# Optimization experiments

Measured on AMD Instinct MI355X. Metric: run time of the kernel, lower is better.

The kernel has to match this reference:

```python
import jax, jax.numpy as jnp
import numpy as np

ALPHA = 0.5
BETA = 0.25
D_AGG = 0.5          # delta_aggregation
D_DIS = 3.0          # delta_discrimination
OHEM_RATIO = 3.0
MAX_INST = 8         # max instance label (labels in 1..MAX_INST, 0 = background)
SMOOTH = 1e-3


def _aggr_discr(text, kernel, embed):
    # text, kernel: [HW] int32 instance labels; embed: [4, HW] float
    inst = jnp.arange(1, MAX_INST + 1)                              # [I]
    kmask = (kernel[None, :] == inst[:, None]).astype(embed.dtype)  # [I, HW]
    tmask = (text[None, :] == inst[:, None]).astype(embed.dtype)   # [I, HW]
    kcnt = kmask.sum(1)                                             # [I]
    tcnt = tmask.sum(1)
    valid = ((kcnt > 0) & (tcnt > 0)).astype(embed.dtype)           # [I]
    # per-instance kernel-mean embedding (segment mean)
    avgs = (kmask @ embed.T) / jnp.maximum(kcnt, 1.0)[:, None]      # [I, 4]
    # aggregation: per-pixel distance to the mean of its text instance
    avgs_full = jnp.concatenate([jnp.zeros((1, 4), embed.dtype), avgs], 0)  # row 0 = bg
    pix_avg = avgs_full[text]                                       # [HW, 4]
    sq = jnp.sum((embed.T - pix_avg) ** 2, axis=1)
    dist = jnp.sqrt(sq + 1e-12) - D_AGG
    lg = jnp.log1p(jnp.maximum(dist, 0.0) ** 2)                     # [HW]
    aggr_i = (tmask @ lg) / jnp.maximum(tcnt, 1.0)                  # [I]
    n = valid.sum()
    loss_aggr = jnp.where(n > 0, (aggr_i * valid).sum() / jnp.maximum(n, 1.0), 0.0)
    # discrimination: pairwise hinge between valid kernel means
    pairv = jnp.triu(valid[:, None] * valid[None, :], k=1)          # [I, I]
    sq_ij = jnp.sum((avgs[:, None, :] - avgs[None, :, :]) ** 2, axis=-1)
    d_ij = jnp.sqrt(jnp.where(pairv > 0, sq_ij, 1.0))               # safe sqrt
    L = jnp.log1p(jnp.maximum(D_DIS - d_ij, 0.0) ** 2)
    denom = n * (n - 1)
    loss_discr = jnp.where(n > 1, (L * pairv).sum() / jnp.maximum(denom, 1.0), 0.0)
    return loss_aggr, loss_discr


def _ohem(score, gt_text, gt_mask):
    # score, gt_text, gt_mask: [HW] float
    pos = gt_text > 0.5
    maskpos = gt_mask > 0.5
    pos_num = (pos & maskpos).sum()
    neg = ~pos
    neg_num = jnp.minimum((pos_num * OHEM_RATIO).astype(jnp.int32), neg.sum())
    neg_sc = jnp.where(neg, score, -jnp.inf)
    srt = -jnp.sort(-neg_sc)                                        # descending
    thr = srt[jnp.clip(neg_num - 1, 0, score.shape[0] - 1)]
    samp = ((score >= thr) | pos) & maskpos
    fallback = (pos_num == 0) | (neg_num == 0)
    return jnp.where(fallback, maskpos, samp).astype(score.dtype)


def _dice(pred_logits, target, mask):
    # all [N, HW]
    p = jax.nn.sigmoid(pred_logits) * mask
    t = (target > 0.5).astype(p.dtype) * mask
    a = jnp.sum(p * t, 1) + SMOOTH
    b = jnp.sum(p * p, 1) + SMOOTH
    c = jnp.sum(t * t, 1) + SMOOTH
    return 1.0 - 2.0 * a / (b + c)


def reference(preds, gt_texts, gt_kernels, gt_mask):
    N, C, H, W = preds.shape
    HW = H * W
    pred_text = preds[:, 0].reshape(N, HW)
    pred_kernel = preds[:, 1].reshape(N, HW)
    embed = preds[:, 2:].reshape(N, 4, HW)
    t = gt_texts.reshape(N, HW)
    k = gt_kernels.reshape(N, HW)
    m = gt_mask.reshape(N, HW).astype(preds.dtype)
    tf = t.astype(preds.dtype)
    kf = k.astype(preds.dtype)
    loss_aggr, loss_discr = jax.vmap(_aggr_discr)(t, k, embed)
    samp = jax.vmap(_ohem)(jax.lax.stop_gradient(pred_text), tf, m)
    loss_text = _dice(pred_text, tf, samp)
    samp_k = (tf > 0.5).astype(preds.dtype) * m
    loss_kernel = _dice(pred_kernel, kf, samp_k)
    # reduction='mean' then coefs [1, alpha, beta, beta]
    return jnp.stack([
        loss_text.mean(),
        ALPHA * loss_kernel.mean(),
        BETA * loss_aggr.mean(),
        BETA * loss_discr.mean(),
    ])


def setup_inputs() -> dict:
    key = jax.random.key(0)
    k1, k2, k3, k4 = jax.random.split(key, 4)
    N, H, W = 16, 512, 512
    preds = jax.random.normal(k1, (N, 6, H, W), dtype=jnp.float32)
    gt_texts = jax.random.randint(k2, (N, H, W), 0, 9, dtype=jnp.int32)
    gt_kernels = jax.random.randint(k3, (N, H, W), 0, 9, dtype=jnp.int32)
    gt_mask = jax.random.randint(k4, (N, H, W), 0, 2, dtype=jnp.int32)
    return {"preds": preds, "gt_texts": gt_texts, "gt_kernels": gt_kernels, "gt_mask": gt_mask}
```

## Files before the change

### kernel.cpp

```cpp
#include <hip/hip_runtime.h>
#include <math.h>

#define HW (512 * 512)
#define NB 16
#define NTHR 256
#define GXS 64
#define CH 4
#define NSEG 256
#define SEGSZ 1024
#define REP 16

#define OFF_ACC    0
#define ACC_STRIDE (NB * 52)
#define OFF_PACC   (OFF_ACC + REP * ACC_STRIDE)
#define PACC_STRIDE (NB * 4)
#define OFF_HISTFB (OFF_PACC + REP * PACC_STRIDE)
#define OFF_NEGMX  (OFF_HISTFB + 4 * 16 * 256)
#define ZERO_WORDS (OFF_NEGMX + NB * REP)
#define OFF_TBL    ZERO_WORDS
#define OFF_THR    (OFF_TBL + 16 * 45)
#define OFF_FB     (OFF_THR + 16)
#define OFF_NVAL   (OFF_FB + 16)
#define OFF_DISCR  (OFF_NVAL + 16)
#define OFF_PREFIX (OFF_DISCR + 16)
#define OFF_KKC    (OFF_PREFIX + 16)
#define OFF_NEGC   (OFF_KKC + 16)
#define OFF_CNTS   (OFF_NEGC + 16)
#define OFF_KEYS   (OFF_CNTS + NB * NSEG)
#define WS_FULL_BYTES ((size_t)(OFF_KEYS + NB * HW) * 4)


__device__ __forceinline__ unsigned fmap(float f) {
    unsigned u = __float_as_uint(f);
    return (u & 0x80000000u) ? ~u : (u | 0x80000000u);
}
__device__ __forceinline__ float funmap(unsigned u) {
    return (u & 0x80000000u) ? __uint_as_float(u & 0x7FFFFFFFu)
                             : __uint_as_float(~u);
}
__device__ __forceinline__ float wred(float x) {
#pragma unroll
    for (int o = 32; o; o >>= 1) x += __shfl_xor(x, o);
    return x;
}
__device__ __forceinline__ unsigned wredu(unsigned x) {
#pragma unroll
    for (int o = 32; o; o >>= 1) x += __shfl_xor(x, o);
    return x;
}
__device__ __forceinline__ unsigned wredumax(unsigned x) {
#pragma unroll
    for (int o = 32; o; o >>= 1) x = max(x, (unsigned)__shfl_xor((int)x, o));
    return x;
}

__global__ __launch_bounds__(NTHR, 2) void k_stats(const float* __restrict__ preds,
                        const int* __restrict__ text,
                        const int* __restrict__ kern,
                        const int* __restrict__ mask,
                        unsigned* __restrict__ wsu, int do_compact) {
    float* wsf = (float*)wsu;
    const int b = blockIdx.y;
    const int tid = threadIdx.x;
    const int lane = tid & 63;
    const unsigned long long lmask = (1ull << lane) - 1ull;
    __shared__ float sacc[52];
    if (tid < 52) sacc[tid] = 0.f;
    __syncthreads();

    const int* tb = text + b * HW;
    const int* kb = kern + b * HW;
    const int* mb = mask + b * HW;
    const float* p0 = preds + (size_t)(b * 6 + 0) * HW;
    const float* p1 = preds + (size_t)(b * 6 + 1) * HW;
    const float* e0 = preds + (size_t)(b * 6 + 2) * HW;
    const float* e1 = e0 + HW;
    const float* e2 = e0 + 2 * HW;
    const float* e3 = e0 + 3 * HW;

    const int seg = blockIdx.x * 4 + (tid >> 6);
    unsigned* keys = wsu + OFF_KEYS + (size_t)b * HW + (size_t)seg * SEGSZ;
    unsigned segoff = 0;
    unsigned mkAll = 0u;

    float ks[32];
#pragma unroll
    for (int i = 0; i < 32; i++) ks[i] = 0.f;
    float r_ak = 0.f, r_bk = 0.f, r_ck = 0.f;
    unsigned kcW[8] = {0, 0, 0, 0, 0, 0, 0, 0};
    unsigned tcW[8] = {0, 0, 0, 0, 0, 0, 0, 0};
    unsigned posW = 0;

#pragma unroll 1
    for (int c = 0; c < CH; c++) {
        const int base = blockIdx.x * (NTHR * 4 * CH) + c * (NTHR * 4) + tid * 4;
        const int4 t4 = *(const int4*)(tb + base);
        const int4 k4 = *(const int4*)(kb + base);
        const int4 m4 = *(const int4*)(mb + base);
        const float4 s4 = *(const float4*)(p0 + base);
        const float4 q4 = *(const float4*)(p1 + base);
        const float4 a4 = *(const float4*)(e0 + base);
        const float4 b4 = *(const float4*)(e1 + base);
        const float4 c4 = *(const float4*)(e2 + base);
        const float4 d4 = *(const float4*)(e3 + base);

#define PIX(T, K, M, Q, A, B, C, D) do {                                     \
        bool pos_ = (T) > 0, mp_ = (M) > 0;                                  \
        float sm_ = (pos_ && mp_) ? 1.f : 0.f;                               \
        float sg_ = 1.f / (1.f + expf(-(Q)));                                \
        float ik_ = ((K) > 0) ? 1.f : 0.f;                                   \
        r_ak += sm_ * sg_ * ik_;                                             \
        r_bk += sm_ * sg_ * sg_;                                             \
        r_ck += sm_ * ik_;                                                   \
        posW += (unsigned)__popcll(__ballot(pos_ && mp_));                   \
        _Pragma("unroll")                                                    \
        for (int i_ = 0; i_ < 8; i_++) {                                     \
            bool hit_ = ((K) == i_ + 1);                                     \
            kcW[i_] += (unsigned)__popcll(__ballot(hit_));                   \
            tcW[i_] += (unsigned)__popcll(__ballot((T) == i_ + 1));          \
            float h_ = hit_ ? 1.f : 0.f;                                     \
            ks[i_ * 4 + 0] += h_ * (A);                                      \
            ks[i_ * 4 + 1] += h_ * (B);                                      \
            ks[i_ * 4 + 2] += h_ * (C);                                      \
            ks[i_ * 4 + 3] += h_ * (D);                                      \
        }                                                                    \
    } while (0)

        PIX(t4.x, k4.x, m4.x, q4.x, a4.x, b4.x, c4.x, d4.x);
        PIX(t4.y, k4.y, m4.y, q4.y, a4.y, b4.y, c4.y, d4.y);
        PIX(t4.z, k4.z, m4.z, q4.z, a4.z, b4.z, c4.z, d4.z);
        PIX(t4.w, k4.w, m4.w, q4.w, a4.w, b4.w, c4.w, d4.w);
#undef PIX

        const unsigned long long m0 = __ballot(t4.x == 0);
        const unsigned long long m1 = __ballot(t4.y == 0);
        const unsigned long long m2 = __ballot(t4.z == 0);
        const unsigned long long m3 = __ballot(t4.w == 0);
        const unsigned c0 = (unsigned)__popcll(m0), c1 = (unsigned)__popcll(m1);
        const unsigned c2 = (unsigned)__popcll(m2), c3 = (unsigned)__popcll(m3);
        if (do_compact) {
            if (t4.x == 0) keys[segoff + (unsigned)__popcll(m0 & lmask)] = fmap(s4.x);
            if (t4.y == 0) keys[segoff + c0 + (unsigned)__popcll(m1 & lmask)] = fmap(s4.y);
            if (t4.z == 0) keys[segoff + c0 + c1 + (unsigned)__popcll(m2 & lmask)] = fmap(s4.z);
            if (t4.w == 0) keys[segoff + c0 + c1 + c2 + (unsigned)__popcll(m3 & lmask)] = fmap(s4.w);
        }
        segoff += c0 + c1 + c2 + c3;
        unsigned mk = 0u;
        if (t4.x == 0) mk = max(mk, ~fmap(s4.x));
        if (t4.y == 0) mk = max(mk, ~fmap(s4.y));
        if (t4.z == 0) mk = max(mk, ~fmap(s4.z));
        if (t4.w == 0) mk = max(mk, ~fmap(s4.w));
        mkAll = max(mkAll, mk);
    }

    if (lane == 0) wsu[OFF_CNTS + b * NSEG + seg] = segoff;
    mkAll = wredumax(mkAll);
    if (lane == 0 && mkAll)
        atomicMax(&wsu[OFF_NEGMX + b * REP + (blockIdx.x & (REP - 1))], mkAll);

#pragma unroll
    for (int i = 0; i < 32; i++) {
        float v = wred(ks[i]);
        if (lane == 0) atomicAdd(&sacc[16 + i], v);
    }
    {
        float v = wred(r_ak); if (lane == 0) atomicAdd(&sacc[49], v);
        v = wred(r_bk); if (lane == 0) atomicAdd(&sacc[50], v);
        v = wred(r_ck); if (lane == 0) atomicAdd(&sacc[51], v);
    }
    if (lane == 0) {
#pragma unroll
        for (int i = 0; i < 8; i++) {
            atomicAdd(&sacc[i], (float)kcW[i]);
            atomicAdd(&sacc[8 + i], (float)tcW[i]);
        }
        atomicAdd(&sacc[48], (float)posW);
    }
    __syncthreads();
    if (tid < 52) {
        const int rep = blockIdx.x & (REP - 1);
        atomicAdd(&wsf[OFF_ACC + rep * ACC_STRIDE + b * 52 + tid], sacc[tid]);
    }
}

__global__ void k_sel(unsigned* __restrict__ wsu, int do_select) {
    float* wsf = (float*)wsu;
    const int b = blockIdx.x;
    const int tid = threadIdx.x;
    const int lane = tid & 63;
    __shared__ float s_acc[52];
    __shared__ float s_avg[8][4];
    __shared__ int s_valid[8];
    __shared__ unsigned s_hist[256];
    __shared__ unsigned s_negtot;
    __shared__ unsigned s_kk, s_prefix;

    if (tid < 52) {
        float v = 0.f;
#pragma unroll
        for (int r = 0; r < REP; r++) v += wsf[OFF_ACC + r * ACC_STRIDE + b * 52 + tid];
        s_acc[tid] = v;
    }
    if (tid == 0) s_negtot = 0u;
    __syncthreads();

    const unsigned myc = wsu[OFF_CNTS + b * NSEG + tid];
    {
        unsigned cw = wredu(myc);
        if (lane == 0) atomicAdd(&s_negtot, cw);
    }
    if (tid < 8) {
        float kcf = s_acc[tid];
        float tcf = s_acc[8 + tid];
        int valid = (kcf > 0.f && tcf > 0.f) ? 1 : 0;
        float inv = 1.f / fmaxf(kcf, 1.f);
        float w = valid ? 1.f / fmaxf(tcf, 1.f) : 0.f;
#pragma unroll
        for (int c = 0; c < 4; c++) {
            float a = s_acc[16 + tid * 4 + c] * inv;
            s_avg[tid][c] = a;
            wsf[OFF_TBL + b * 45 + (tid + 1) * 5 + c] = a;
        }
        s_valid[tid] = valid;
        wsf[OFF_TBL + b * 45 + (tid + 1) * 5 + 4] = w;
    }
    if (tid >= 8 && tid < 13) wsf[OFF_TBL + b * 45 + (tid - 8)] = 0.f;
    __syncthreads();
    if (tid == 0) {
        int nval = 0;
        for (int i = 0; i < 8; i++) nval += s_valid[i];
        float L = 0.f;
        for (int i = 0; i < 8; i++)
            for (int j = i + 1; j < 8; j++)
                if (s_valid[i] && s_valid[j]) {
                    float sq = 0.f;
                    for (int c = 0; c < 4; c++) {
                        float d = s_avg[i][c] - s_avg[j][c];
                        sq += d * d;
                    }
                    float h = fmaxf(3.0f - sqrtf(sq), 0.f);
                    L += log1pf(h * h);
                }
        wsf[OFF_DISCR + b] = (nval > 1) ? L / fmaxf((float)(nval * (nval - 1)), 1.f) : 0.f;
        wsu[OFF_NVAL + b] = (unsigned)nval;
        unsigned pos = (unsigned)s_acc[48];
        unsigned neg = s_negtot;
        wsu[OFF_NEGC + b] = neg;
        unsigned nn = min(pos * 3u, neg);
        int fb = (pos == 0u || nn == 0u) ? 1 : 0;
        wsu[OFF_FB + b] = (unsigned)fb;
        wsu[OFF_KKC + b] = fb ? 0u : nn;
        wsu[OFF_PREFIX + b] = 0u;
        wsf[OFF_THR + b] = 0.f;
        unsigned kk = fb ? 0u : nn;
        if (!fb && nn == neg) {
            unsigned mx = 0u;
#pragma unroll
            for (int r = 0; r < REP; r++) mx = max(mx, wsu[OFF_NEGMX + b * REP + r]);
            wsf[OFF_THR + b] = funmap(~mx);
            kk = 0u;
        }
        s_kk = kk;
        s_prefix = 0u;
    }
    __syncthreads();
    if (!do_select) return;
    if (s_kk == 0u) return;
    const unsigned* keys = wsu + OFF_KEYS + (size_t)b * HW + (size_t)tid * SEGSZ;
    unsigned prefix = 0u;
    for (int pass = 0; pass < 4; pass++) {
        const int shift = 24 - 8 * pass;
        const unsigned fmask = (pass == 0) ? 0u : (0xFFFFFFFFu << (shift + 8));
        s_hist[tid] = 0u;
        __syncthreads();
        for (unsigned i = 0; i < myc; i++) {
            unsigned key = keys[i];
            if ((key & fmask) == prefix) atomicAdd(&s_hist[(key >> shift) & 255u], 1u);
        }
        __syncthreads();
        if (tid == 0) {
            unsigned k2 = s_kk;
            for (int bin = 255; bin >= 0; --bin) {
                unsigned c = s_hist[bin];
                if (k2 <= c) { s_prefix = prefix | (((unsigned)bin) << shift); s_kk = k2; break; }
                k2 -= c;
            }
        }
        __syncthreads();
        prefix = s_prefix;
    }
    if (tid == 0) wsf[OFF_THR + b] = funmap(prefix);
}

__global__ void k_hist(const float* __restrict__ preds, const int* __restrict__ text,
                       unsigned* __restrict__ wsu, int pass) {
    const int b = blockIdx.y;
    const int tid = threadIdx.x;
    __shared__ unsigned h[256];
    h[tid] = 0u;
    __syncthreads();
    const unsigned prefix = wsu[OFF_PREFIX + b];
    const int shift = 24 - 8 * pass;
    const unsigned fmask = (pass == 0) ? 0u : (0xFFFFFFFFu << (shift + 8));
    const int* tb = text + b * HW;
    const float* pt = preds + (size_t)(b * 6) * HW;
    for (int p = blockIdx.x * NTHR + tid; p < HW; p += gridDim.x * NTHR) {
        if (tb[p] == 0) {
            unsigned key = fmap(pt[p]);
            if ((key & fmask) == prefix) atomicAdd(&h[(key >> shift) & 255u], 1u);
        }
    }
    __syncthreads();
    if (h[tid]) atomicAdd(&wsu[OFF_HISTFB + pass * 4096 + b * 256 + tid], h[tid]);
}
__global__ void k_select(unsigned* __restrict__ wsu, int pass) {
    int b = threadIdx.x;
    if (b >= NB) return;
    float* wsf = (float*)wsu;
    unsigned k = wsu[OFF_KKC + b];
    unsigned prefix = wsu[OFF_PREFIX + b];
    const int shift = 24 - 8 * pass;
    const unsigned* h = &wsu[OFF_HISTFB + pass * 4096 + b * 256];
    if (k > 0) {
        for (int bin = 255; bin >= 0; --bin) {
            unsigned c = h[bin];
            if (k <= c) { prefix |= ((unsigned)bin) << shift; break; }
            k -= c;
        }
        wsu[OFF_KKC + b] = k;
        wsu[OFF_PREFIX + b] = prefix;
    }
    if (pass == 3) wsf[OFF_THR + b] = funmap(prefix);
}

__global__ __launch_bounds__(NTHR, 2) void k_pix(const float* __restrict__ preds,
                      const int* __restrict__ text,
                      const int* __restrict__ mask,
                      unsigned* __restrict__ wsu) {
    float* wsf = (float*)wsu;
    const int b = blockIdx.y;
    const int tid = threadIdx.x;
    const int lane = tid & 63;
    __shared__ float stbl[45];
    __shared__ float sred[4];
    __shared__ float sthr;
    __shared__ unsigned sfb;
    if (tid < 45) stbl[tid] = wsf[OFF_TBL + b * 45 + tid];
    if (tid < 4) sred[tid] = 0.f;
    if (tid == 0) { sthr = wsf[OFF_THR + b]; sfb = wsu[OFF_FB + b]; }
    __syncthreads();
    const float thr = sthr;
    const bool fb = sfb != 0u;
    float r_at = 0.f, r_bt = 0.f, r_ct = 0.f, r_ag = 0.f;
    const int* tb = text + b * HW;
    const int* mb = mask + b * HW;
    const float* p0 = preds + (size_t)(b * 6) * HW;
    const float* e0 = preds + (size_t)(b * 6 + 2) * HW;
    const float* e1 = e0 + HW;
    const float* e2 = e0 + 2 * HW;
    const float* e3 = e0 + 3 * HW;

#pragma unroll 1
    for (int c = 0; c < CH; c++) {
        const int base = blockIdx.x * (NTHR * 4 * CH) + c * (NTHR * 4) + tid * 4;
        const int4 t4 = *(const int4*)(tb + base);
        const int4 m4 = *(const int4*)(mb + base);
        const float4 s4 = *(const float4*)(p0 + base);
        const float4 a4 = *(const float4*)(e0 + base);
        const float4 b4 = *(const float4*)(e1 + base);
        const float4 c4 = *(const float4*)(e2 + base);
        const float4 d4 = *(const float4*)(e3 + base);

#define PPIX(T, M, S, A, B, C, D) do {                                       \
        bool pos_ = (T) > 0;                                                 \
        bool samp_ = fb ? ((M) > 0) : ((((S) >= thr) || pos_) && ((M) > 0)); \
        float sg_ = 1.f / (1.f + expf(-(S)));                                \
        float smf_ = samp_ ? 1.f : 0.f;                                      \
        float it_ = pos_ ? 1.f : 0.f;                                        \
        r_at += smf_ * sg_ * it_;                                            \
        r_bt += smf_ * sg_ * sg_;                                            \
        r_ct += smf_ * it_;                                                  \
        int t5_ = min((T), 8) * 5;                                           \
        float d0_ = (A) - stbl[t5_ + 0];                                     \
        float d1_ = (B) - stbl[t5_ + 1];                                     \
        float d2_ = (C) - stbl[t5_ + 2];                                     \
        float d3_ = (D) - stbl[t5_ + 3];                                     \
        float w_ = stbl[t5_ + 4];                                            \
        float sq_ = d0_ * d0_ + d1_ * d1_ + d2_ * d2_ + d3_ * d3_;           \
        float dist_ = sqrtf(sq_ + 1e-12f) - 0.5f;                            \
        float hp_ = fmaxf(dist_, 0.f);                                       \
        r_ag += w_ * log1pf(hp_ * hp_);                                      \
    } while (0)

        PPIX(t4.x, m4.x, s4.x, a4.x, b4.x, c4.x, d4.x);
        PPIX(t4.y, m4.y, s4.y, a4.y, b4.y, c4.y, d4.y);
        PPIX(t4.z, m4.z, s4.z, a4.z, b4.z, c4.z, d4.z);
        PPIX(t4.w, m4.w, s4.w, a4.w, b4.w, c4.w, d4.w);
#undef PPIX
    }

    {
        float v = wred(r_at); if (lane == 0) atomicAdd(&sred[0], v);
        v = wred(r_bt); if (lane == 0) atomicAdd(&sred[1], v);
        v = wred(r_ct); if (lane == 0) atomicAdd(&sred[2], v);
        v = wred(r_ag); if (lane == 0) atomicAdd(&sred[3], v);
    }
    __syncthreads();
    if (tid < 4) {
        const int rep = blockIdx.x & (REP - 1);
        atomicAdd(&wsf[OFF_PACC + rep * PACC_STRIDE + b * 4 + tid], sred[tid]);
    }
}

__global__ void k_final(unsigned* __restrict__ wsu, float* __restrict__ out) {
    float* wsf = (float*)wsu;
    __shared__ float lt[NB], lk[NB], la[NB], ld[NB];
    int b = threadIdx.x;
    if (b < NB) {
        const float S = 1e-3f;
        float ak = 0.f, bk = 0.f, ck = 0.f, at = 0.f, bt = 0.f, ct = 0.f, ag = 0.f;
#pragma unroll
        for (int r = 0; r < REP; r++) {
            ak += wsf[OFF_ACC + r * ACC_STRIDE + b * 52 + 49];
            bk += wsf[OFF_ACC + r * ACC_STRIDE + b * 52 + 50];
            ck += wsf[OFF_ACC + r * ACC_STRIDE + b * 52 + 51];
            at += wsf[OFF_PACC + r * PACC_STRIDE + b * 4 + 0];
            bt += wsf[OFF_PACC + r * PACC_STRIDE + b * 4 + 1];
            ct += wsf[OFF_PACC + r * PACC_STRIDE + b * 4 + 2];
            ag += wsf[OFF_PACC + r * PACC_STRIDE + b * 4 + 3];
        }
        lt[b] = 1.f - 2.f * (at + S) / ((bt + S) + (ct + S));
        lk[b] = 1.f - 2.f * (ak + S) / ((bk + S) + (ck + S));
        int nval = (int)wsu[OFF_NVAL + b];
        la[b] = (nval > 0) ? ag / fmaxf((float)nval, 1.f) : 0.f;
        ld[b] = wsf[OFF_DISCR + b];
    }
    __syncthreads();
    if (b == 0) {
        float st = 0, sk = 0, sa = 0, sd = 0;
        for (int i = 0; i < NB; i++) { st += lt[i]; sk += lk[i]; sa += la[i]; sd += ld[i]; }
        out[0] = st / NB;
        out[1] = 0.5f * sk / NB;
        out[2] = 0.25f * sa / NB;
        out[3] = 0.25f * sd / NB;
    }
}

extern "C" void kernel_launch(void* const* d_in, const int* in_sizes, int n_in,
                              void* d_out, int out_size, void* d_ws, size_t ws_size,
                              hipStream_t stream) {
    const float* preds = (const float*)d_in[0];
    const int* text = (const int*)d_in[1];
    const int* kern = (const int*)d_in[2];
    const int* mask = (const int*)d_in[3];
    unsigned* wsu = (unsigned*)d_ws;
    float* out = (float*)d_out;

    const int do_compact = (ws_size >= WS_FULL_BYTES) ? 1 : 0;

    hipMemsetAsync(d_ws, 0, (size_t)ZERO_WORDS * 4, stream);

    dim3 grid(GXS, NB);
    k_stats<<<grid, NTHR, 0, stream>>>(preds, text, kern, mask, wsu, do_compact);
    k_sel<<<NB, NTHR, 0, stream>>>(wsu, do_compact);
    if (!do_compact) {
        dim3 hgrid(128, NB);
        for (int pass = 0; pass < 4; pass++) {
            k_hist<<<hgrid, NTHR, 0, stream>>>(preds, text, wsu, pass);
            k_select<<<1, 64, 0, stream>>>(wsu, pass);
        }
    }
    k_pix<<<grid, NTHR, 0, stream>>>(preds, text, mask, wsu);
    k_final<<<1, 64, 0, stream>>>(wsu, out);
}
```

Before: 244.7 us.

## Drop memset and final kernel, use per-block partials and last-block finalize

Removes the workspace memset and the separate k_final launch. k_stats now writes per-block partials that k_sel reduces, and k_sel zeroes the k_pix accumulators. k_pix finishes the loss in the last block, found with an atomic ticket counter. The main loops now work on int2/float2 chunks with software double-buffered loads, launch bounds are raised to 4 blocks per SM, and text-instance counts use a packed 64-bit counter instead of ballots. This trades launch overhead and ballot work for more register pressure and a threadfence-plus-atomic finalize path.

```diff
diff --git a/kernel.cpp b/kernel.cpp
--- a/kernel.cpp
+++ b/kernel.cpp
@@ -5,27 +5,26 @@
 #define NB 16
 #define NTHR 256
 #define GXS 64
-#define CH 4
+#define CH2 8
 #define NSEG 256
 #define SEGSZ 1024
-#define REP 16
+#define PREP 4
 
 #define OFF_ACC    0
-#define ACC_STRIDE (NB * 52)
-#define OFF_PACC   (OFF_ACC + REP * ACC_STRIDE)
-#define PACC_STRIDE (NB * 4)
-#define OFF_HISTFB (OFF_PACC + REP * PACC_STRIDE)
-#define OFF_NEGMX  (OFF_HISTFB + 4 * 16 * 256)
-#define ZERO_WORDS (OFF_NEGMX + NB * REP)
-#define OFF_TBL    ZERO_WORDS
-#define OFF_THR    (OFF_TBL + 16 * 45)
-#define OFF_FB     (OFF_THR + 16)
-#define OFF_NVAL   (OFF_FB + 16)
-#define OFF_DISCR  (OFF_NVAL + 16)
-#define OFF_PREFIX (OFF_DISCR + 16)
-#define OFF_KKC    (OFF_PREFIX + 16)
-#define OFF_NEGC   (OFF_KKC + 16)
-#define OFF_CNTS   (OFF_NEGC + 16)
+#define OFF_NEGMX  (OFF_ACC + NB * GXS * 52)
+#define OFF_PACC   (OFF_NEGMX + NB * GXS)
+#define OFF_TICK   (OFF_PACC + PREP * NB * 4)
+#define OFF_KDICE  (OFF_TICK + 16)
+#define OFF_TBL    (OFF_KDICE + NB * 3)
+#define OFF_THR    (OFF_TBL + NB * 45)
+#define OFF_FB     (OFF_THR + NB)
+#define OFF_NVAL   (OFF_FB + NB)
+#define OFF_DISCR  (OFF_NVAL + NB)
+#define OFF_PREFIX (OFF_DISCR + NB)
+#define OFF_KKC    (OFF_PREFIX + NB)
+#define OFF_NEGC   (OFF_KKC + NB)
+#define OFF_HISTFB (OFF_NEGC + NB)
+#define OFF_CNTS   (OFF_HISTFB + 4 * 16 * 256)
 #define OFF_KEYS   (OFF_CNTS + NB * NSEG)
 #define WS_FULL_BYTES ((size_t)(OFF_KEYS + NB * HW) * 4)
 
@@ -53,8 +52,14 @@
     for (int o = 32; o; o >>= 1) x = max(x, (unsigned)__shfl_xor((int)x, o));
     return x;
 }
-
-__global__ __launch_bounds__(NTHR, 2) void k_stats(const float* __restrict__ preds,
+__device__ __forceinline__ unsigned long long wredull(unsigned long long x) {
+#pragma unroll
+    for (int o = 32; o; o >>= 1)
+        x += (unsigned long long)__shfl_xor((unsigned long long)x, o);
+    return x;
+}
+
+__global__ __launch_bounds__(NTHR, 4) void k_stats(const float* __restrict__ preds,
                         const int* __restrict__ text,
                         const int* __restrict__ kern,
                         const int* __restrict__ mask,
@@ -65,7 +70,9 @@
     const int lane = tid & 63;
     const unsigned long long lmask = (1ull << lane) - 1ull;
     __shared__ float sacc[52];
+    __shared__ unsigned smx;
     if (tid < 52) sacc[tid] = 0.f;
+    if (tid == 0) smx = 0u;
     __syncthreads();
 
     const int* tb = text + b * HW;
@@ -86,23 +93,24 @@
     float ks[32];
 #pragma unroll
     for (int i = 0; i < 32; i++) ks[i] = 0.f;
-    float r_ak = 0.f, r_bk = 0.f, r_ck = 0.f;
+    float r_ak = 0.f, r_bk = 0.f, r_ck = 0.f, r_pos = 0.f;
     unsigned kcW[8] = {0, 0, 0, 0, 0, 0, 0, 0};
-    unsigned tcW[8] = {0, 0, 0, 0, 0, 0, 0, 0};
-    unsigned posW = 0;
-
-#pragma unroll 1
-    for (int c = 0; c < CH; c++) {
-        const int base = blockIdx.x * (NTHR * 4 * CH) + c * (NTHR * 4) + tid * 4;
-        const int4 t4 = *(const int4*)(tb + base);
-        const int4 k4 = *(const int4*)(kb + base);
-        const int4 m4 = *(const int4*)(mb + base);
-        const float4 s4 = *(const float4*)(p0 + base);
-        const float4 q4 = *(const float4*)(p1 + base);
-        const float4 a4 = *(const float4*)(e0 + base);
-        const float4 b4 = *(const float4*)(e1 + base);
-        const float4 c4 = *(const float4*)(e2 + base);
-        const float4 d4 = *(const float4*)(e3 + base);
+    unsigned long long tpack = 0ull;
+
+#define BASE_(ci_) (blockIdx.x * (NTHR * 16) + ((ci_) >> 1) * (NTHR * 4) + ((ci_) & 1) * 2 + tid * 4)
+
+#define LOADC(P, ci_) do {                                                   \
+        const int base_ = BASE_(ci_);                                        \
+        P##t = *(const int2*)(tb + base_);                                   \
+        P##k = *(const int2*)(kb + base_);                                   \
+        P##m = *(const int2*)(mb + base_);                                   \
+        P##s = *(const float2*)(p0 + base_);                                 \
+        P##q = *(const float2*)(p1 + base_);                                 \
+        P##a = *(const float2*)(e0 + base_);                                 \
+        P##b = *(const float2*)(e1 + base_);                                 \
+        P##c = *(const float2*)(e2 + base_);                                 \
+        P##d = *(const float2*)(e3 + base_);                                 \
+    } while (0)
 
 #define PIX(T, K, M, Q, A, B, C, D) do {                                     \
         bool pos_ = (T) > 0, mp_ = (M) > 0;                                  \
@@ -112,12 +120,12 @@
         r_ak += sm_ * sg_ * ik_;                                             \
         r_bk += sm_ * sg_ * sg_;                                             \
         r_ck += sm_ * ik_;                                                   \
-        posW += (unsigned)__popcll(__ballot(pos_ && mp_));                   \
+        r_pos += sm_;                                                        \
+        tpack += pos_ ? (1ull << ((((unsigned)(T) - 1u) & 7u) * 8u)) : 0ull; \
         _Pragma("unroll")                                                    \
         for (int i_ = 0; i_ < 8; i_++) {                                     \
             bool hit_ = ((K) == i_ + 1);                                     \
             kcW[i_] += (unsigned)__popcll(__ballot(hit_));                   \
-            tcW[i_] += (unsigned)__popcll(__ballot((T) == i_ + 1));          \
             float h_ = hit_ ? 1.f : 0.f;                                     \
             ks[i_ * 4 + 0] += h_ * (A);                                      \
             ks[i_ * 4 + 1] += h_ * (B);                                      \
@@ -126,37 +134,45 @@
         }                                                                    \
     } while (0)
 
-        PIX(t4.x, k4.x, m4.x, q4.x, a4.x, b4.x, c4.x, d4.x);
-        PIX(t4.y, k4.y, m4.y, q4.y, a4.y, b4.y, c4.y, d4.y);
-        PIX(t4.z, k4.z, m4.z, q4.z, a4.z, b4.z, c4.z, d4.z);
-        PIX(t4.w, k4.w, m4.w, q4.w, a4.w, b4.w, c4.w, d4.w);
+#define PROC(P) do {                                                            \
+        PIX(P##t.x, P##k.x, P##m.x, P##q.x, P##a.x, P##b.x, P##c.x, P##d.x);    \
+        PIX(P##t.y, P##k.y, P##m.y, P##q.y, P##a.y, P##b.y, P##c.y, P##d.y);    \
+        const unsigned long long m0_ = __ballot(P##t.x == 0);                   \
+        const unsigned long long m1_ = __ballot(P##t.y == 0);                   \
+        const unsigned c0_ = (unsigned)__popcll(m0_);                           \
+        const unsigned c1_ = (unsigned)__popcll(m1_);                           \
+        if (do_compact) {                                                       \
+            if (P##t.x == 0)                                                    \
+                keys[segoff + (unsigned)__popcll(m0_ & lmask)] = fmap(P##s.x);  \
+            if (P##t.y == 0)                                                    \
+                keys[segoff + c0_ + (unsigned)__popcll(m1_ & lmask)] = fmap(P##s.y); \
+        }                                                                       \
+        segoff += c0_ + c1_;                                                    \
+        unsigned mk_ = 0u;                                                      \
+        if (P##t.x == 0) mk_ = max(mk_, ~fmap(P##s.x));                         \
+        if (P##t.y == 0) mk_ = max(mk_, ~fmap(P##s.y));                         \
+        mkAll = max(mkAll, mk_);                                                \
+    } while (0)
+
+    int2 At, Ak, Am;  float2 As, Aq, Aa, Ab, Ac, Ad;
+    int2 Bt, Bk, Bm;  float2 Bs, Bq, Ba, Bb, Bc, Bd;
+
+    LOADC(A, 0);
+#pragma unroll 1
+    for (int cc = 0; cc < CH2 / 2; ++cc) {
+        LOADC(B, cc * 2 + 1);
+        PROC(A);
+        if (cc + 1 < CH2 / 2) LOADC(A, cc * 2 + 2);
+        PROC(B);
+    }
+#undef PROC
 #undef PIX
-
-        const unsigned long long m0 = __ballot(t4.x == 0);
-        const unsigned long long m1 = __ballot(t4.y == 0);
-        const unsigned long long m2 = __ballot(t4.z == 0);
-        const unsigned long long m3 = __ballot(t4.w == 0);
-        const unsigned c0 = (unsigned)__popcll(m0), c1 = (unsigned)__popcll(m1);
-        const unsigned c2 = (unsigned)__popcll(m2), c3 = (unsigned)__popcll(m3);
-        if (do_compact) {
-            if (t4.x == 0) keys[segoff + (unsigned)__popcll(m0 & lmask)] = fmap(s4.x);
-            if (t4.y == 0) keys[segoff + c0 + (unsigned)__popcll(m1 & lmask)] = fmap(s4.y);
-            if (t4.z == 0) keys[segoff + c0 + c1 + (unsigned)__popcll(m2 & lmask)] = fmap(s4.z);
-            if (t4.w == 0) keys[segoff + c0 + c1 + c2 + (unsigned)__popcll(m3 & lmask)] = fmap(s4.w);
-        }
-        segoff += c0 + c1 + c2 + c3;
-        unsigned mk = 0u;
-        if (t4.x == 0) mk = max(mk, ~fmap(s4.x));
-        if (t4.y == 0) mk = max(mk, ~fmap(s4.y));
-        if (t4.z == 0) mk = max(mk, ~fmap(s4.z));
-        if (t4.w == 0) mk = max(mk, ~fmap(s4.w));
-        mkAll = max(mkAll, mk);
-    }
+#undef LOADC
+#undef BASE_
 
     if (lane == 0) wsu[OFF_CNTS + b * NSEG + seg] = segoff;
     mkAll = wredumax(mkAll);
-    if (lane == 0 && mkAll)
-        atomicMax(&wsu[OFF_NEGMX + b * REP + (blockIdx.x & (REP - 1))], mkAll);
+    if (lane == 0) atomicMax(&smx, mkAll);
 
 #pragma unroll
     for (int i = 0; i < 32; i++) {
@@ -167,20 +183,33 @@
         float v = wred(r_ak); if (lane == 0) atomicAdd(&sacc[49], v);
         v = wred(r_bk); if (lane == 0) atomicAdd(&sacc[50], v);
         v = wred(r_ck); if (lane == 0) atomicAdd(&sacc[51], v);
+        v = wred(r_pos); if (lane == 0) atomicAdd(&sacc[48], v);
+    }
+    {
+        unsigned long long lo = tpack & 0x00FF00FF00FF00FFull;
+        unsigned long long hi = (tpack >> 8) & 0x00FF00FF00FF00FFull;
+        lo = wredull(lo);
+        hi = wredull(hi);
+        if (lane == 0) {
+            atomicAdd(&sacc[8 + 0], (float)(unsigned)( lo        & 0xFFFFull));
+            atomicAdd(&sacc[8 + 2], (float)(unsigned)((lo >> 16) & 0xFFFFull));
+            atomicAdd(&sacc[8 + 4], (float)(unsigned)((lo >> 32) & 0xFFFFull));
+            atomicAdd(&sacc[8 + 6], (float)(unsigned)((lo >> 48) & 0xFFFFull));
+            atomicAdd(&sacc[8 + 1], (float)(unsigned)( hi        & 0xFFFFull));
+            atomicAdd(&sacc[8 + 3], (float)(unsigned)((hi >> 16) & 0xFFFFull));
+            atomicAdd(&sacc[8 + 5], (float)(unsigned)((hi >> 32) & 0xFFFFull));
+            atomicAdd(&sacc[8 + 7], (float)(unsigned)((hi >> 48) & 0xFFFFull));
+        }
     }
     if (lane == 0) {
 #pragma unroll
-        for (int i = 0; i < 8; i++) {
-            atomicAdd(&sacc[i], (float)kcW[i]);
-            atomicAdd(&sacc[8 + i], (float)tcW[i]);
-        }
-        atomicAdd(&sacc[48], (float)posW);
-    }
-    __syncthreads();
-    if (tid < 52) {
-        const int rep = blockIdx.x & (REP - 1);
-        atomicAdd(&wsf[OFF_ACC + rep * ACC_STRIDE + b * 52 + tid], sacc[tid]);
-    }
+        for (int i = 0; i < 8; i++) atomicAdd(&sacc[i], (float)kcW[i]);
+    }
+    __syncthreads();
+    if (tid < 52)
+        wsf[OFF_ACC + (b * GXS + blockIdx.x) * 52 + tid] = sacc[tid];
+    if (tid == 0)
+        wsu[OFF_NEGMX + b * GXS + blockIdx.x] = smx;
 }
 
 __global__ void k_sel(unsigned* __restrict__ wsu, int do_select) {
@@ -193,21 +222,32 @@
     __shared__ int s_valid[8];
     __shared__ unsigned s_hist[256];
     __shared__ unsigned s_negtot;
+    __shared__ unsigned s_negmax;
     __shared__ unsigned s_kk, s_prefix;
 
     if (tid < 52) {
         float v = 0.f;
-#pragma unroll
-        for (int r = 0; r < REP; r++) v += wsf[OFF_ACC + r * ACC_STRIDE + b * 52 + tid];
+        const float* p = wsf + OFF_ACC + b * GXS * 52 + tid;
+#pragma unroll 8
+        for (int r = 0; r < GXS; r++) v += p[r * 52];
         s_acc[tid] = v;
     }
     if (tid == 0) s_negtot = 0u;
+    if (b == 0) {
+        if (tid < PREP * NB * 4) wsf[OFF_PACC + tid] = 0.f;
+        if (tid == 0) wsu[OFF_TICK] = 0u;
+    }
     __syncthreads();
 
     const unsigned myc = wsu[OFF_CNTS + b * NSEG + tid];
     {
         unsigned cw = wredu(myc);
         if (lane == 0) atomicAdd(&s_negtot, cw);
+    }
+    if (tid < 64) {
+        unsigned m = wsu[OFF_NEGMX + b * GXS + tid];
+        m = wredumax(m);
+        if (tid == 0) s_negmax = m;
     }
     if (tid < 8) {
         float kcf = s_acc[tid];
@@ -225,6 +265,7 @@
         wsf[OFF_TBL + b * 45 + (tid + 1) * 5 + 4] = w;
     }
     if (tid >= 8 && tid < 13) wsf[OFF_TBL + b * 45 + (tid - 8)] = 0.f;
+    if (tid >= 16 && tid < 19) wsf[OFF_KDICE + b * 3 + (tid - 16)] = s_acc[49 + (tid - 16)];
     __syncthreads();
     if (tid == 0) {
         int nval = 0;
@@ -254,10 +295,7 @@
         wsf[OFF_THR + b] = 0.f;
         unsigned kk = fb ? 0u : nn;
         if (!fb && nn == neg) {
-            unsigned mx = 0u;
-#pragma unroll
-            for (int r = 0; r < REP; r++) mx = max(mx, wsu[OFF_NEGMX + b * REP + r]);
-            wsf[OFF_THR + b] = funmap(~mx);
+            wsf[OFF_THR + b] = funmap(~s_negmax);
             kk = 0u;
         }
         s_kk = kk;
@@ -333,10 +371,11 @@
     if (pass == 3) wsf[OFF_THR + b] = funmap(prefix);
 }
 
-__global__ __launch_bounds__(NTHR, 2) void k_pix(const float* __restrict__ preds,
+__global__ __launch_bounds__(NTHR, 4) void k_pix(const float* __restrict__ preds,
                       const int* __restrict__ text,
                       const int* __restrict__ mask,
-                      unsigned* __restrict__ wsu) {
+                      unsigned* __restrict__ wsu,
+                      float* __restrict__ out) {
     float* wsf = (float*)wsu;
     const int b = blockIdx.y;
     const int tid = threadIdx.x;
@@ -345,6 +384,9 @@
     __shared__ float sred[4];
     __shared__ float sthr;
     __shared__ unsigned sfb;
+    __shared__ unsigned s_last;
+    __shared__ float sfin[64];
+    __shared__ float lt[NB], lk[NB], la[NB], ld[NB];
     if (tid < 45) stbl[tid] = wsf[OFF_TBL + b * 45 + tid];
     if (tid < 4) sred[tid] = 0.f;
     if (tid == 0) { sthr = wsf[OFF_THR + b]; sfb = wsu[OFF_FB + b]; }
@@ -360,16 +402,17 @@
     const float* e2 = e0 + 2 * HW;
     const float* e3 = e0 + 3 * HW;
 
-#pragma unroll 1
-    for (int c = 0; c < CH; c++) {
-        const int base = blockIdx.x * (NTHR * 4 * CH) + c * (NTHR * 4) + tid * 4;
-        const int4 t4 = *(const int4*)(tb + base);
-        const int4 m4 = *(const int4*)(mb + base);
-        const float4 s4 = *(const float4*)(p0 + base);
-        const float4 a4 = *(const float4*)(e0 + base);
-        const float4 b4 = *(const float4*)(e1 + base);
-        const float4 c4 = *(const float4*)(e2 + base);
-        const float4 d4 = *(const float4*)(e3 + base);
+#define BASE_(ci_) (blockIdx.x * (NTHR * 16) + ((ci_) >> 1) * (NTHR * 4) + ((ci_) & 1) * 2 + tid * 4)
+#define PLOADC(P, ci_) do {                                                  \
+        const int base_ = BASE_(ci_);                                        \
+        P##t = *(const int2*)(tb + base_);                                   \
+        P##m = *(const int2*)(mb + base_);                                   \
+        P##s = *(const float2*)(p0 + base_);                                 \
+        P##a = *(const float2*)(e0 + base_);                                 \
+        P##b = *(const float2*)(e1 + base_);                                 \
+        P##c = *(const float2*)(e2 + base_);                                 \
+        P##d = *(const float2*)(e3 + base_);                                 \
+    } while (0)
 
 #define PPIX(T, M, S, A, B, C, D) do {                                       \
         bool pos_ = (T) > 0;                                                 \
@@ -392,12 +435,26 @@
         r_ag += w_ * log1pf(hp_ * hp_);                                      \
     } while (0)
 
-        PPIX(t4.x, m4.x, s4.x, a4.x, b4.x, c4.x, d4.x);
-        PPIX(t4.y, m4.y, s4.y, a4.y, b4.y, c4.y, d4.y);
-        PPIX(t4.z, m4.z, s4.z, a4.z, b4.z, c4.z, d4.z);
-        PPIX(t4.w, m4.w, s4.w, a4.w, b4.w, c4.w, d4.w);
+#define PPROC(P) do {                                                        \
+        PPIX(P##t.x, P##m.x, P##s.x, P##a.x, P##b.x, P##c.x, P##d.x);        \
+        PPIX(P##t.y, P##m.y, P##s.y, P##a.y, P##b.y, P##c.y, P##d.y);        \
+    } while (0)
+
+    int2 At, Am;  float2 As, Aa, Ab, Ac, Ad;
+    int2 Bt, Bm;  float2 Bs, Ba, Bb, Bc, Bd;
+
+    PLOADC(A, 0);
+#pragma unroll 1
+    for (int cc = 0; cc < CH2 / 2; ++cc) {
+        PLOADC(B, cc * 2 + 1);
+        PPROC(A);
+        if (cc + 1 < CH2 / 2) PLOADC(A, cc * 2 + 2);
+        PPROC(B);
+    }
+#undef PPROC
 #undef PPIX
-    }
+#undef PLOADC
+#undef BASE_
 
     {
         float v = wred(r_at); if (lane == 0) atomicAdd(&sred[0], v);
@@ -407,36 +464,40 @@
     }
     __syncthreads();
     if (tid < 4) {
-        const int rep = blockIdx.x & (REP - 1);
-        atomicAdd(&wsf[OFF_PACC + rep * PACC_STRIDE + b * 4 + tid], sred[tid]);
-    }
-}
-
-__global__ void k_final(unsigned* __restrict__ wsu, float* __restrict__ out) {
-    float* wsf = (float*)wsu;
-    __shared__ float lt[NB], lk[NB], la[NB], ld[NB];
-    int b = threadIdx.x;
-    if (b < NB) {
+        const int rep = blockIdx.x & (PREP - 1);
+        atomicAdd(&wsf[OFF_PACC + (rep * NB + b) * 4 + tid], sred[tid]);
+    }
+    __threadfence();
+    if (tid == 0) {
+        unsigned t = atomicAdd(&wsu[OFF_TICK], 1u);
+        s_last = (t == (unsigned)(GXS * NB - 1)) ? 1u : 0u;
+    }
+    __syncthreads();
+    if (!s_last) return;
+    if (tid < 64) {
+        const int bb = tid >> 2, v = tid & 3;
+        float s = 0.f;
+#pragma unroll
+        for (int r = 0; r < PREP; r++)
+            s += atomicAdd(&wsf[OFF_PACC + (r * NB + bb) * 4 + v], 0.f);
+        sfin[tid] = s;
+    }
+    __syncthreads();
+    if (tid < NB) {
         const float S = 1e-3f;
-        float ak = 0.f, bk = 0.f, ck = 0.f, at = 0.f, bt = 0.f, ct = 0.f, ag = 0.f;
-#pragma unroll
-        for (int r = 0; r < REP; r++) {
-            ak += wsf[OFF_ACC + r * ACC_STRIDE + b * 52 + 49];
-            bk += wsf[OFF_ACC + r * ACC_STRIDE + b * 52 + 50];
-            ck += wsf[OFF_ACC + r * ACC_STRIDE + b * 52 + 51];
-            at += wsf[OFF_PACC + r * PACC_STRIDE + b * 4 + 0];
-            bt += wsf[OFF_PACC + r * PACC_STRIDE + b * 4 + 1];
-            ct += wsf[OFF_PACC + r * PACC_STRIDE + b * 4 + 2];
-            ag += wsf[OFF_PACC + r * PACC_STRIDE + b * 4 + 3];
-        }
-        lt[b] = 1.f - 2.f * (at + S) / ((bt + S) + (ct + S));
-        lk[b] = 1.f - 2.f * (ak + S) / ((bk + S) + (ck + S));
-        int nval = (int)wsu[OFF_NVAL + b];
-        la[b] = (nval > 0) ? ag / fmaxf((float)nval, 1.f) : 0.f;
-        ld[b] = wsf[OFF_DISCR + b];
-    }
-    __syncthreads();
-    if (b == 0) {
+        float at = sfin[tid * 4 + 0], bt = sfin[tid * 4 + 1];
+        float ct = sfin[tid * 4 + 2], ag = sfin[tid * 4 + 3];
+        float ak = wsf[OFF_KDICE + tid * 3 + 0];
+        float bk = wsf[OFF_KDICE + tid * 3 + 1];
+        float ck = wsf[OFF_KDICE + tid * 3 + 2];
+        lt[tid] = 1.f - 2.f * (at + S) / ((bt + S) + (ct + S));
+        lk[tid] = 1.f - 2.f * (ak + S) / ((bk + S) + (ck + S));
+        int nval = (int)wsu[OFF_NVAL + tid];
+        la[tid] = (nval > 0) ? ag / fmaxf((float)nval, 1.f) : 0.f;
+        ld[tid] = wsf[OFF_DISCR + tid];
+    }
+    __syncthreads();
+    if (tid == 0) {
         float st = 0, sk = 0, sa = 0, sd = 0;
         for (int i = 0; i < NB; i++) { st += lt[i]; sk += lk[i]; sa += la[i]; sd += ld[i]; }
         out[0] = st / NB;
@@ -458,18 +519,17 @@
 
     const int do_compact = (ws_size >= WS_FULL_BYTES) ? 1 : 0;
 
-    hipMemsetAsync(d_ws, 0, (size_t)ZERO_WORDS * 4, stream);
-
     dim3 grid(GXS, NB);
     k_stats<<<grid, NTHR, 0, stream>>>(preds, text, kern, mask, wsu, do_compact);
     k_sel<<<NB, NTHR, 0, stream>>>(wsu, do_compact);
     if (!do_compact) {
+        (void)hipMemsetAsync((char*)d_ws + (size_t)OFF_HISTFB * 4, 0,
+                             (size_t)4 * 16 * 256 * 4, stream);
         dim3 hgrid(128, NB);
         for (int pass = 0; pass < 4; pass++) {
             k_hist<<<hgrid, NTHR, 0, stream>>>(preds, text, wsu, pass);
             k_select<<<1, 64, 0, stream>>>(wsu, pass);
         }
     }
-    k_pix<<<grid, NTHR, 0, stream>>>(preds, text, mask, wsu);
-    k_final<<<1, 64, 0, stream>>>(wsu, out);
-}
+    k_pix<<<grid, NTHR, 0, stream>>>(preds, text, mask, wsu, out);
+}
```

Result: slower. 347.0 us (+41.8%).

## Pack per-class counts into bytes, drop memset, write per-block partials

Applied to the files above, without the earlier changes.

Per-pixel ballot/popcount counting of the eight text and kernel classes is replaced by byte-packed 64-bit counters, which are reduced across the wave once at the end. This removes sixteen ballots per pixel and frees registers. The grid doubles to 128 blocks with half the chunks each, and launch bounds are raised so more waves can be resident. Global atomics into replicated accumulators become plain per-block stores that k_sel reduces, and the upfront memset is dropped, with PACC zeroed inside k_sel. The risks are byte-counter overflow if a lane accumulates 256 or more pixels of one class (it only sees 8 pixels here) and a larger reduction in k_sel.

```diff
diff --git a/kernel.cpp b/kernel.cpp
--- a/kernel.cpp
+++ b/kernel.cpp
@@ -4,28 +4,26 @@
 #define HW (512 * 512)
 #define NB 16
 #define NTHR 256
-#define GXS 64
-#define CH 4
-#define NSEG 256
-#define SEGSZ 1024
-#define REP 16
+#define GXS 128
+#define CH 2
+#define NSEG (GXS * 4)
+#define SEGSZ 512
+#define PREP 4
 
 #define OFF_ACC    0
-#define ACC_STRIDE (NB * 52)
-#define OFF_PACC   (OFF_ACC + REP * ACC_STRIDE)
-#define PACC_STRIDE (NB * 4)
-#define OFF_HISTFB (OFF_PACC + REP * PACC_STRIDE)
-#define OFF_NEGMX  (OFF_HISTFB + 4 * 16 * 256)
-#define ZERO_WORDS (OFF_NEGMX + NB * REP)
-#define OFF_TBL    ZERO_WORDS
-#define OFF_THR    (OFF_TBL + 16 * 45)
-#define OFF_FB     (OFF_THR + 16)
-#define OFF_NVAL   (OFF_FB + 16)
-#define OFF_DISCR  (OFF_NVAL + 16)
-#define OFF_PREFIX (OFF_DISCR + 16)
-#define OFF_KKC    (OFF_PREFIX + 16)
-#define OFF_NEGC   (OFF_KKC + 16)
-#define OFF_CNTS   (OFF_NEGC + 16)
+#define OFF_NEGMX  (OFF_ACC + NB * GXS * 52)
+#define OFF_PACC   (OFF_NEGMX + NB * GXS)
+#define OFF_KDICE  (OFF_PACC + PREP * NB * 4)
+#define OFF_TBL    (OFF_KDICE + NB * 3)
+#define OFF_THR    (OFF_TBL + NB * 45)
+#define OFF_FB     (OFF_THR + NB)
+#define OFF_NVAL   (OFF_FB + NB)
+#define OFF_DISCR  (OFF_NVAL + NB)
+#define OFF_PREFIX (OFF_DISCR + NB)
+#define OFF_KKC    (OFF_PREFIX + NB)
+#define OFF_NEGC   (OFF_KKC + NB)
+#define OFF_HISTFB (OFF_NEGC + NB)
+#define OFF_CNTS   (OFF_HISTFB + 4 * 16 * 256)
 #define OFF_KEYS   (OFF_CNTS + NB * NSEG)
 #define WS_FULL_BYTES ((size_t)(OFF_KEYS + NB * HW) * 4)
 
@@ -53,8 +51,14 @@
     for (int o = 32; o; o >>= 1) x = max(x, (unsigned)__shfl_xor((int)x, o));
     return x;
 }
-
-__global__ __launch_bounds__(NTHR, 2) void k_stats(const float* __restrict__ preds,
+__device__ __forceinline__ unsigned long long wredull(unsigned long long x) {
+#pragma unroll
+    for (int o = 32; o; o >>= 1)
+        x += (unsigned long long)__shfl_xor((unsigned long long)x, o);
+    return x;
+}
+
+__global__ __launch_bounds__(NTHR, 4) void k_stats(const float* __restrict__ preds,
                         const int* __restrict__ text,
                         const int* __restrict__ kern,
                         const int* __restrict__ mask,
@@ -65,7 +69,9 @@
     const int lane = tid & 63;
     const unsigned long long lmask = (1ull << lane) - 1ull;
     __shared__ float sacc[52];
+    __shared__ unsigned smx;
     if (tid < 52) sacc[tid] = 0.f;
+    if (tid == 0) smx = 0u;
     __syncthreads();
 
     const int* tb = text + b * HW;
@@ -86,10 +92,9 @@
     float ks[32];
 #pragma unroll
     for (int i = 0; i < 32; i++) ks[i] = 0.f;
-    float r_ak = 0.f, r_bk = 0.f, r_ck = 0.f;
-    unsigned kcW[8] = {0, 0, 0, 0, 0, 0, 0, 0};
-    unsigned tcW[8] = {0, 0, 0, 0, 0, 0, 0, 0};
-    unsigned posW = 0;
+    float r_ak = 0.f, r_bk = 0.f, r_ck = 0.f, r_pos = 0.f;
+    unsigned long long tpack = 0ull;
+    unsigned long long kpack = 0ull;
 
 #pragma unroll 1
     for (int c = 0; c < CH; c++) {
@@ -112,13 +117,12 @@
         r_ak += sm_ * sg_ * ik_;                                             \
         r_bk += sm_ * sg_ * sg_;                                             \
         r_ck += sm_ * ik_;                                                   \
-        posW += (unsigned)__popcll(__ballot(pos_ && mp_));                   \
+        r_pos += sm_;                                                        \
+        tpack += pos_ ? (1ull << ((((unsigned)(T) - 1u) & 7u) * 8u)) : 0ull; \
+        kpack += ((K) > 0) ? (1ull << ((((unsigned)(K) - 1u) & 7u) * 8u)) : 0ull; \
         _Pragma("unroll")                                                    \
         for (int i_ = 0; i_ < 8; i_++) {                                     \
-            bool hit_ = ((K) == i_ + 1);                                     \
-            kcW[i_] += (unsigned)__popcll(__ballot(hit_));                   \
-            tcW[i_] += (unsigned)__popcll(__ballot((T) == i_ + 1));          \
-            float h_ = hit_ ? 1.f : 0.f;                                     \
+            float h_ = ((K) == i_ + 1) ? 1.f : 0.f;                          \
             ks[i_ * 4 + 0] += h_ * (A);                                      \
             ks[i_ * 4 + 1] += h_ * (B);                                      \
             ks[i_ * 4 + 2] += h_ * (C);                                      \
@@ -155,8 +159,7 @@
 
     if (lane == 0) wsu[OFF_CNTS + b * NSEG + seg] = segoff;
     mkAll = wredumax(mkAll);
-    if (lane == 0 && mkAll)
-        atomicMax(&wsu[OFF_NEGMX + b * REP + (blockIdx.x & (REP - 1))], mkAll);
+    if (lane == 0) atomicMax(&smx, mkAll);
 
 #pragma unroll
     for (int i = 0; i < 32; i++) {
@@ -167,20 +170,41 @@
         float v = wred(r_ak); if (lane == 0) atomicAdd(&sacc[49], v);
         v = wred(r_bk); if (lane == 0) atomicAdd(&sacc[50], v);
         v = wred(r_ck); if (lane == 0) atomicAdd(&sacc[51], v);
-    }
-    if (lane == 0) {
-#pragma unroll
-        for (int i = 0; i < 8; i++) {
-            atomicAdd(&sacc[i], (float)kcW[i]);
-            atomicAdd(&sacc[8 + i], (float)tcW[i]);
-        }
-        atomicAdd(&sacc[48], (float)posW);
-    }
-    __syncthreads();
-    if (tid < 52) {
-        const int rep = blockIdx.x & (REP - 1);
-        atomicAdd(&wsf[OFF_ACC + rep * ACC_STRIDE + b * 52 + tid], sacc[tid]);
-    }
+        v = wred(r_pos); if (lane == 0) atomicAdd(&sacc[48], v);
+    }
+    {
+        unsigned long long lo = tpack & 0x00FF00FF00FF00FFull;
+        unsigned long long hi = (tpack >> 8) & 0x00FF00FF00FF00FFull;
+        lo = wredull(lo);
+        hi = wredull(hi);
+        unsigned long long klo = kpack & 0x00FF00FF00FF00FFull;
+        unsigned long long khi = (kpack >> 8) & 0x00FF00FF00FF00FFull;
+        klo = wredull(klo);
+        khi = wredull(khi);
+        if (lane == 0) {
+            atomicAdd(&sacc[8 + 0], (float)(unsigned)( lo        & 0xFFFFull));
+            atomicAdd(&sacc[8 + 2], (float)(unsigned)((lo >> 16) & 0xFFFFull));
+            atomicAdd(&sacc[8 + 4], (float)(unsigned)((lo >> 32) & 0xFFFFull));
+            atomicAdd(&sacc[8 + 6], (float)(unsigned)((lo >> 48) & 0xFFFFull));
+            atomicAdd(&sacc[8 + 1], (float)(unsigned)( hi        & 0xFFFFull));
+            atomicAdd(&sacc[8 + 3], (float)(unsigned)((hi >> 16) & 0xFFFFull));
+            atomicAdd(&sacc[8 + 5], (float)(unsigned)((hi >> 32) & 0xFFFFull));
+            atomicAdd(&sacc[8 + 7], (float)(unsigned)((hi >> 48) & 0xFFFFull));
+            atomicAdd(&sacc[0], (float)(unsigned)( klo        & 0xFFFFull));
+            atomicAdd(&sacc[2], (float)(unsigned)((klo >> 16) & 0xFFFFull));
+            atomicAdd(&sacc[4], (float)(unsigned)((klo >> 32) & 0xFFFFull));
+            atomicAdd(&sacc[6], (float)(unsigned)((klo >> 48) & 0xFFFFull));
+            atomicAdd(&sacc[1], (float)(unsigned)( khi        & 0xFFFFull));
+            atomicAdd(&sacc[3], (float)(unsigned)((khi >> 16) & 0xFFFFull));
+            atomicAdd(&sacc[5], (float)(unsigned)((khi >> 32) & 0xFFFFull));
+            atomicAdd(&sacc[7], (float)(unsigned)((khi >> 48) & 0xFFFFull));
+        }
+    }
+    __syncthreads();
+    if (tid < 52)
+        wsf[OFF_ACC + (b * GXS + blockIdx.x) * 52 + tid] = sacc[tid];
+    if (tid == 0)
+        wsu[OFF_NEGMX + b * GXS + blockIdx.x] = smx;
 }
 
 __global__ void k_sel(unsigned* __restrict__ wsu, int do_select) {
@@ -193,21 +217,30 @@
     __shared__ int s_valid[8];
     __shared__ unsigned s_hist[256];
     __shared__ unsigned s_negtot;
+    __shared__ unsigned s_negmax;
     __shared__ unsigned s_kk, s_prefix;
 
     if (tid < 52) {
         float v = 0.f;
-#pragma unroll
-        for (int r = 0; r < REP; r++) v += wsf[OFF_ACC + r * ACC_STRIDE + b * 52 + tid];
+        const float* p = wsf + OFF_ACC + b * GXS * 52 + tid;
+#pragma unroll 8
+        for (int r = 0; r < GXS; r++) v += p[r * 52];
         s_acc[tid] = v;
     }
-    if (tid == 0) s_negtot = 0u;
-    __syncthreads();
-
-    const unsigned myc = wsu[OFF_CNTS + b * NSEG + tid];
+    if (tid == 0) { s_negtot = 0u; s_negmax = 0u; }
+    if (b == 0 && tid < PREP * NB * 4) wsf[OFF_PACC + tid] = 0.f;
+    __syncthreads();
+
+    const unsigned myc0 = wsu[OFF_CNTS + b * NSEG + tid];
+    const unsigned myc1 = wsu[OFF_CNTS + b * NSEG + tid + 256];
     {
-        unsigned cw = wredu(myc);
+        unsigned cw = wredu(myc0 + myc1);
         if (lane == 0) atomicAdd(&s_negtot, cw);
+    }
+    if (tid < GXS) {
+        unsigned m = wsu[OFF_NEGMX + b * GXS + tid];
+        m = wredumax(m);
+        if (lane == 0) atomicMax(&s_negmax, m);
     }
     if (tid < 8) {
         float kcf = s_acc[tid];
@@ -225,6 +258,7 @@
         wsf[OFF_TBL + b * 45 + (tid + 1) * 5 + 4] = w;
     }
     if (tid >= 8 && tid < 13) wsf[OFF_TBL + b * 45 + (tid - 8)] = 0.f;
+    if (tid >= 16 && tid < 19) wsf[OFF_KDICE + b * 3 + (tid - 16)] = s_acc[49 + (tid - 16)];
     __syncthreads();
     if (tid == 0) {
         int nval = 0;
@@ -254,10 +288,7 @@
         wsf[OFF_THR + b] = 0.f;
         unsigned kk = fb ? 0u : nn;
         if (!fb && nn == neg) {
-            unsigned mx = 0u;
-#pragma unroll
-            for (int r = 0; r < REP; r++) mx = max(mx, wsu[OFF_NEGMX + b * REP + r]);
-            wsf[OFF_THR + b] = funmap(~mx);
+            wsf[OFF_THR + b] = funmap(~s_negmax);
             kk = 0u;
         }
         s_kk = kk;
@@ -266,15 +297,20 @@
     __syncthreads();
     if (!do_select) return;
     if (s_kk == 0u) return;
-    const unsigned* keys = wsu + OFF_KEYS + (size_t)b * HW + (size_t)tid * SEGSZ;
+    const unsigned* keys0 = wsu + OFF_KEYS + (size_t)b * HW + (size_t)tid * SEGSZ;
+    const unsigned* keys1 = keys0 + (size_t)256 * SEGSZ;
     unsigned prefix = 0u;
     for (int pass = 0; pass < 4; pass++) {
         const int shift = 24 - 8 * pass;
         const unsigned fmask = (pass == 0) ? 0u : (0xFFFFFFFFu << (shift + 8));
         s_hist[tid] = 0u;
         __syncthreads();
-        for (unsigned i = 0; i < myc; i++) {
-            unsigned key = keys[i];
+        for (unsigned i = 0; i < myc0; i++) {
+            unsigned key = keys0[i];
+            if ((key & fmask) == prefix) atomicAdd(&s_hist[(key >> shift) & 255u], 1u);
+        }
+        for (unsigned i = 0; i < myc1; i++) {
+            unsigned key = keys1[i];
             if ((key & fmask) == prefix) atomicAdd(&s_hist[(key >> shift) & 255u], 1u);
         }
         __syncthreads();
@@ -333,7 +369,7 @@
     if (pass == 3) wsf[OFF_THR + b] = funmap(prefix);
 }
 
-__global__ __launch_bounds__(NTHR, 2) void k_pix(const float* __restrict__ preds,
+__global__ __launch_bounds__(NTHR, 4) void k_pix(const float* __restrict__ preds,
                       const int* __restrict__ text,
                       const int* __restrict__ mask,
                       unsigned* __restrict__ wsu) {
@@ -407,8 +443,8 @@
     }
     __syncthreads();
     if (tid < 4) {
-        const int rep = blockIdx.x & (REP - 1);
-        atomicAdd(&wsf[OFF_PACC + rep * PACC_STRIDE + b * 4 + tid], sred[tid]);
+        const int rep = blockIdx.x & (PREP - 1);
+        atomicAdd(&wsf[OFF_PACC + (rep * NB + b) * 4 + tid], sred[tid]);
     }
 }
 
@@ -418,17 +454,17 @@
     int b = threadIdx.x;
     if (b < NB) {
         const float S = 1e-3f;
-        float ak = 0.f, bk = 0.f, ck = 0.f, at = 0.f, bt = 0.f, ct = 0.f, ag = 0.f;
-#pragma unroll
-        for (int r = 0; r < REP; r++) {
-            ak += wsf[OFF_ACC + r * ACC_STRIDE + b * 52 + 49];
-            bk += wsf[OFF_ACC + r * ACC_STRIDE + b * 52 + 50];
-            ck += wsf[OFF_ACC + r * ACC_STRIDE + b * 52 + 51];
-            at += wsf[OFF_PACC + r * PACC_STRIDE + b * 4 + 0];
-            bt += wsf[OFF_PACC + r * PACC_STRIDE + b * 4 + 1];
-            ct += wsf[OFF_PACC + r * PACC_STRIDE + b * 4 + 2];
-            ag += wsf[OFF_PACC + r * PACC_STRIDE + b * 4 + 3];
-        }
+        float at = 0.f, bt = 0.f, ct = 0.f, ag = 0.f;
+#pragma unroll
+        for (int r = 0; r < PREP; r++) {
+            at += wsf[OFF_PACC + (r * NB + b) * 4 + 0];
+            bt += wsf[OFF_PACC + (r * NB + b) * 4 + 1];
+            ct += wsf[OFF_PACC + (r * NB + b) * 4 + 2];
+            ag += wsf[OFF_PACC + (r * NB + b) * 4 + 3];
+        }
+        float ak = wsf[OFF_KDICE + b * 3 + 0];
+        float bk = wsf[OFF_KDICE + b * 3 + 1];
+        float ck = wsf[OFF_KDICE + b * 3 + 2];
         lt[b] = 1.f - 2.f * (at + S) / ((bt + S) + (ct + S));
         lk[b] = 1.f - 2.f * (ak + S) / ((bk + S) + (ck + S));
         int nval = (int)wsu[OFF_NVAL + b];
@@ -458,12 +494,12 @@
 
     const int do_compact = (ws_size >= WS_FULL_BYTES) ? 1 : 0;
 
-    hipMemsetAsync(d_ws, 0, (size_t)ZERO_WORDS * 4, stream);
-
     dim3 grid(GXS, NB);
     k_stats<<<grid, NTHR, 0, stream>>>(preds, text, kern, mask, wsu, do_compact);
     k_sel<<<NB, NTHR, 0, stream>>>(wsu, do_compact);
     if (!do_compact) {
+        (void)hipMemsetAsync((char*)d_ws + (size_t)OFF_HISTFB * 4, 0,
+                             (size_t)4 * 16 * 256 * 4, stream);
         dim3 hgrid(128, NB);
         for (int pass = 0; pass < 4; pass++) {
             k_hist<<<hgrid, NTHR, 0, stream>>>(preds, text, wsu, pass);
```

Result: slower. 265.8 us (+8.6%).
